# Optimization experiments

Measured on AMD Instinct MI355X. Metric: run time of the kernel, lower is better.

Reference implementation:

```python
import math
import jax, jax.numpy as jnp
import numpy as np

B, SX, SY, D, H = 2, 1024, 1024, 1024, 16
FULL = 1536   # padded (full_q == full_k) frame length for the two-source attention
N_CTX = 2048  # causal bias buffer size
HD = D // H
LENS_X = np.array([1024, 700])
LENS_Y = np.array([1024, 850])


def _heads(t):
    b, s, d = t.shape
    return t.reshape(b, s, H, HD).transpose(0, 2, 1, 3)  # [B,H,S,HD]


def _merge(t):
    b, h, s, hd = t.shape
    return t.transpose(0, 2, 1, 3).reshape(b, s, h * hd)


def setup_inputs() -> dict:
    key = jax.random.key(0)
    ks = jax.random.split(key, 8)
    s = 0.02
    # ragged pack/unpack index lists: take = positions in the FULL frame, fill = positions in the shrunk frame
    x_take_b = np.concatenate([np.full(l, b, np.int32) for b, l in enumerate(LENS_X)])
    x_take_p = np.concatenate([(FULL - l + np.arange(l)).astype(np.int32) for l in LENS_X])  # right-aligned
    x_fill_b = x_take_b.copy()
    x_fill_p = np.concatenate([np.arange(l, dtype=np.int32) for l in LENS_X])
    y_take_b = np.concatenate([np.full(l, b, np.int32) for b, l in enumerate(LENS_Y)])
    y_take_p = np.concatenate([np.arange(l, dtype=np.int32) for l in LENS_Y])  # left-aligned
    y_fill_b = y_take_b.copy()
    y_fill_p = y_take_p.copy()
    # additive padding mask for the self-attention over shrunk x
    mask = np.full((B, 1, 1, SX), -10000.0, np.float32)
    for b, l in enumerate(LENS_X):
        mask[b, :, :, :l] = 0.0
    return {
        "x": jax.random.normal(ks[0], (B, SX, D), jnp.float32),
        "y": jax.random.normal(ks[1], (B, SY, D), jnp.float32),
        "attention_mask_x": jnp.asarray(mask),
        "W_attn": jax.random.normal(ks[2], (D, 3 * D), jnp.float32) * s,
        "b_attn": jnp.zeros((3 * D,), jnp.float32),
        "W_2a": jax.random.normal(ks[3], (D, D), jnp.float32) * s,
        "b_2a": jnp.zeros((D,), jnp.float32),
        "W_2b": jax.random.normal(ks[4], (D, 2 * D), jnp.float32) * s,
        "b_2b": jnp.zeros((2 * D,), jnp.float32),
        "W_proj": jax.random.normal(ks[5], (2 * D, D), jnp.float32) * s,
        "b_proj": jnp.zeros((D,), jnp.float32),
        "x_take_b": jnp.asarray(x_take_b), "x_take_p": jnp.asarray(x_take_p),
        "x_fill_b": jnp.asarray(x_fill_b), "x_fill_p": jnp.asarray(x_fill_p),
        "y_take_b": jnp.asarray(y_take_b), "y_take_p": jnp.asarray(y_take_p),
        "y_fill_b": jnp.asarray(y_fill_b), "y_fill_p": jnp.asarray(y_fill_p),
    }


def reference(x, y, attention_mask_x, W_attn, b_attn, W_2a, b_2a, W_2b, b_2b,
              W_proj, b_proj, x_take_b, x_take_p, x_fill_b, x_fill_p,
              y_take_b, y_take_p, y_fill_b, y_fill_p):
    causal = jnp.tril(jnp.ones((N_CTX, N_CTX), jnp.float32))
    inv_sqrt = 1.0 / math.sqrt(HD)

    # --- branch 1: causal self-attention on shrunk x ---
    qkv = x @ W_attn + b_attn
    q, k, v = jnp.split(qkv, 3, axis=2)
    q, k, v = _heads(q), _heads(k), _heads(v)
    w = jnp.einsum('bhqd,bhkd->bhqk', q, k) * inv_sqrt  # [B,H,SX,SX]
    b1 = causal[:SX, :SX]
    w = w * b1 - 10000.0 * (1.0 - b1) + attention_mask_x
    a = jnp.einsum('bhqk,bhkd->bhqd', jax.nn.softmax(w, axis=-1), v)
    a = _merge(a)  # [B,SX,D]

    # --- branch 2: two-source attention with ragged expand/shrink ---
    q2 = _heads(x @ W_2a + b_2a)                      # [B,H,SX,HD]
    k2, v2 = jnp.split(y @ W_2b + b_2b, 2, axis=2)
    k2, v2 = _heads(k2), _heads(v2)                   # [B,H,SY,HD]
    w2 = jnp.einsum('bhqd,bhkd->bhqk', q2, k2)        # [B,H,SX,SY] (unscaled yet)
    # expand key dim: shrunk SY -> FULL
    temp = jnp.zeros((B, H, SX, FULL), w2.dtype)
    temp = temp.at[y_take_b, :, :, y_take_p].set(w2[y_fill_b, :, :, y_fill_p])
    # expand query dim: shrunk SX -> FULL
    new_w = jnp.zeros((B, H, FULL, FULL), w2.dtype)
    new_w = new_w.at[x_take_b, :, x_take_p, :].set(temp[x_fill_b, :, x_fill_p, :])
    new_v = jnp.zeros((B, H, FULL, HD), v2.dtype)
    new_v = new_v.at[y_take_b, :, y_take_p, :].set(v2[y_fill_b, :, y_fill_p, :])
    kmask = jnp.full((B, 1, 1, FULL), -10000.0, w2.dtype)
    kmask = kmask.at[y_take_b, :, :, y_take_p].set(0.0)
    new_w = new_w * inv_sqrt
    b2 = causal[:FULL, :FULL]  # ns-nd == 0 since full_q == full_k
    new_w = new_w * b2 - 10000.0 * (1.0 - b2) + kmask
    a2 = jnp.einsum('bhqk,bhkd->bhqd', jax.nn.softmax(new_w, axis=-1), new_v)  # [B,H,FULL,HD]
    # shrink query dim back: FULL -> SX
    a2s = jnp.zeros((B, H, SX, HD), a2.dtype)
    a2s = a2s.at[x_fill_b, :, x_fill_p, :].set(a2[x_take_b, :, x_take_p, :])
    a2m = _merge(a2s)  # [B,SX,D]

    out = jnp.concatenate([a, a2m], axis=2) @ W_proj + b_proj  # [B,SX,D]
    return out
```

## Files before the change

### kernel.cpp

```cpp
#include <hip/hip_runtime.h>
#include <hip/hip_bf16.h>

typedef __bf16 bf16;
typedef __attribute__((ext_vector_type(4))) __bf16 bf16x4;
typedef __attribute__((ext_vector_type(8))) __bf16 bf16x8;
typedef __attribute__((ext_vector_type(4))) float floatx4;

__device__ __forceinline__ void gl_lds16(const bf16* g, bf16* l) {
  __builtin_amdgcn_global_load_lds(
      (const __attribute__((address_space(1))) void*)g,
      (__attribute__((address_space(3))) void*)l, 16, 0, 0);
}

__global__ __launch_bounds__(256) void sentinel_kernel(float* out, int n, float code) {
  int i = blockIdx.x * 256 + threadIdx.x;
  if (i < n) out[i] = code;
}

struct TP { const float* W; bf16* WT; int K; int N; int bxn; int bid0; };

__global__ __launch_bounds__(256) void prep_kernel(TP t0, TP t1, TP t2, TP t3,
                                                   const float* __restrict__ x,
                                                   const float* __restrict__ y,
                                                   bf16* __restrict__ xb,
                                                   bf16* __restrict__ yb) {
  int bid = blockIdx.x;
  int tid = threadIdx.x;
  if (bid < 2048) {
    __shared__ float tile[64][65];
    TP t = t0;
    if (bid >= t3.bid0) t = t3;
    else if (bid >= t2.bid0) t = t2;
    else if (bid >= t1.bid0) t = t1;
    int rb = bid - t.bid0;
    int n0 = (rb % t.bxn) * 64, k0 = (rb / t.bxn) * 64;
    int tx = tid & 15, ty = tid >> 4;
#pragma unroll
    for (int i = 0; i < 4; ++i) {
      floatx4 v = *(const floatx4*)(t.W + (size_t)(k0 + ty + 16 * i) * t.N + n0 + tx * 4);
#pragma unroll
      for (int j = 0; j < 4; ++j) tile[ty + 16 * i][tx * 4 + j] = v[j];
    }
    __syncthreads();
#pragma unroll
    for (int i = 0; i < 4; ++i) {
      int nr = ty + 16 * i;
      bf16x4 o;
#pragma unroll
      for (int j = 0; j < 4; ++j) o[j] = (bf16)tile[tx * 4 + j][nr];
      *(bf16x4*)(t.WT + (size_t)(n0 + nr) * t.K + k0 + tx * 4) = o;
    }
  } else {
    long base = (long)(bid - 2048) * 4096 + (long)tid * 16;
    const float* src = x; bf16* dst = xb; long idx = base;
    if (base >= 2097152) { src = y; dst = yb; idx = base - 2097152; }
    floatx4 v0 = *(const floatx4*)(src + idx);
    floatx4 v1 = *(const floatx4*)(src + idx + 4);
    floatx4 v2 = *(const floatx4*)(src + idx + 8);
    floatx4 v3 = *(const floatx4*)(src + idx + 12);
    bf16x8 o0, o1;
#pragma unroll
    for (int i = 0; i < 4; ++i) {
      o0[i] = (bf16)v0[i]; o0[4 + i] = (bf16)v1[i];
      o1[i] = (bf16)v2[i]; o1[4 + i] = (bf16)v3[i];
    }
    *(bf16x8*)(dst + idx) = o0;
    *(bf16x8*)(dst + idx + 8) = o1;
  }
}

struct GP { const bf16* A; const bf16* WT; const float* bias; bf16* C; bf16* VT;
            int N; int ldc; int vcol0; int bxn; int bid0; };

__global__ __launch_bounds__(256, 3) void proj3_kernel(GP g0, GP g1, GP g2) {
  __shared__ __attribute__((aligned(16))) bf16 As[128 * 64];
  __shared__ __attribute__((aligned(16))) bf16 Bs[128 * 64];
  int rawb = blockIdx.x;
  int bid = (rawb & 7) * 96 + (rawb >> 3);
  GP g = g0;
  if (bid >= g2.bid0) g = g2;
  else if (bid >= g1.bid0) g = g1;
  int rb = bid - g.bid0;
  int row0 = (rb / g.bxn) * 128, col0 = (rb % g.bxn) * 128;
  int tid = threadIdx.x;
  int lane = tid & 63, wave = tid >> 6;
  int quad = lane >> 4, l16 = lane & 15;
  int wm = wave >> 1, wn = wave & 1;
  const bf16* Ag = g.A + (size_t)row0 * 1024;
  const bf16* Bg = g.WT + (size_t)col0 * 1024;

  floatx4 acc[4][4] = {};

  for (int k0 = 0; k0 < 1024; k0 += 64) {
#pragma unroll
    for (int s = 0; s < 4; ++s) {
      int sl = s * 256 + tid;
      int r = sl >> 3, o = sl & 7;
      int c = (o ^ (r & 7)) * 8;
      gl_lds16(Ag + (size_t)r * 1024 + k0 + c, As + (size_t)sl * 8);
      gl_lds16(Bg + (size_t)r * 1024 + k0 + c, Bs + (size_t)sl * 8);
    }
    __syncthreads();
#pragma unroll
    for (int kk = 0; kk < 2; ++kk) {
      int ko = kk * 4 + quad;
      bf16x8 afr[4], bfr[4];
#pragma unroll
      for (int r = 0; r < 4; ++r) {
        int m = wm * 64 + r * 16 + l16;
        afr[r] = *(const bf16x8*)(As + (size_t)(m * 8 + (ko ^ (m & 7))) * 8);
      }
#pragma unroll
      for (int c = 0; c < 4; ++c) {
        int n = wn * 64 + c * 16 + l16;
        bfr[c] = *(const bf16x8*)(Bs + (size_t)(n * 8 + (ko ^ (n & 7))) * 8);
      }
#pragma unroll
      for (int r = 0; r < 4; ++r)
#pragma unroll
        for (int c = 0; c < 4; ++c)
          acc[r][c] = __builtin_amdgcn_mfma_f32_16x16x32_bf16(afr[r], bfr[c], acc[r][c], 0, 0, 0);
    }
    __syncthreads();
  }

  int inV = (col0 >= g.vcol0);
  if (inV) {
#pragma unroll
    for (int c = 0; c < 4; ++c) {
      int gcol = col0 + wn * 64 + c * 16 + l16;
      float bv = g.bias[gcol];
      int vcol = gcol - g.vcol0;
      int hh = vcol >> 6, dd = vcol & 63;
#pragma unroll
      for (int r = 0; r < 4; ++r) {
        int row = row0 + wm * 64 + r * 16 + quad * 4;
        int bb = row >> 10, key = row & 1023;
        bf16x4 pk;
#pragma unroll
        for (int e = 0; e < 4; ++e) pk[e] = (bf16)(acc[r][c][e] + bv);
        *(bf16x4*)(g.VT + ((size_t)((bb << 4) + hh)) * 65536 + (size_t)dd * 1024 + key) = pk;
      }
    }
  } else {
    bf16* S = ((bf16*)As) + wave * 1152;
    float bvv[4];
#pragma unroll
    for (int c = 0; c < 4; ++c) bvv[c] = g.bias[col0 + wn * 64 + c * 16 + l16];
#pragma unroll
    for (int r = 0; r < 4; ++r) {
#pragma unroll
      for (int c = 0; c < 4; ++c)
#pragma unroll
        for (int e = 0; e < 4; ++e)
          S[(quad * 4 + e) * 72 + c * 16 + l16] = (bf16)(acc[r][c][e] + bvv[c]);
      asm volatile("s_waitcnt lgkmcnt(0)" ::: "memory");
      int R0 = row0 + wm * 64 + r * 16;
#pragma unroll
      for (int t = 0; t < 2; ++t) {
        int s = t * 64 + lane;
        int rr = s >> 3, q = s & 7;
        bf16x8 vv = *(const bf16x8*)(S + rr * 72 + q * 8);
        *(bf16x8*)(g.C + (size_t)(R0 + rr) * g.ldc + col0 + wn * 64 + q * 8) = vv;
      }
      asm volatile("s_waitcnt lgkmcnt(0)" ::: "memory");
    }
  }
}

__global__ __launch_bounds__(256) void gemm_out_kernel(const bf16* __restrict__ A,
                                                       const bf16* __restrict__ WT,
                                                       const float* __restrict__ bias,
                                                       float* __restrict__ C) {
  const int K = 2048;
  __shared__ __attribute__((aligned(16))) bf16 As[128 * 64];
  __shared__ __attribute__((aligned(16))) bf16 Bs[64 * 64];
  int raw = blockIdx.x;
  int bid = (raw & 7) * 32 + (raw >> 3);
  int row0 = (bid >> 4) * 128;
  int col0 = (bid & 15) * 64;
  int tid = threadIdx.x;
  int lane = tid & 63, wave = tid >> 6;
  int quad = lane >> 4, l16 = lane & 15;
  int wm = wave >> 1, wn = wave & 1;
  floatx4 acc[4][2] = {};
  for (int k0 = 0; k0 < K; k0 += 64) {
#pragma unroll
    for (int s = 0; s < 4; ++s) {
      int sl = s * 256 + tid;
      int r = sl >> 3, o = sl & 7;
      int c = (o ^ (r & 7)) * 8;
      gl_lds16(A + (size_t)(row0 + r) * K + k0 + c, As + (size_t)sl * 8);
      if (s < 2)
        gl_lds16(WT + (size_t)(col0 + r) * K + k0 + c, Bs + (size_t)sl * 8);
    }
    __syncthreads();
#pragma unroll
    for (int kk = 0; kk < 2; ++kk) {
      int ko = kk * 4 + quad;
      bf16x8 afr[4], bfr[2];
#pragma unroll
      for (int r = 0; r < 4; ++r) {
        int m = wm * 64 + r * 16 + l16;
        afr[r] = *(const bf16x8*)(As + (size_t)(m * 8 + (ko ^ (m & 7))) * 8);
      }
#pragma unroll
      for (int c = 0; c < 2; ++c) {
        int n = wn * 32 + c * 16 + l16;
        bfr[c] = *(const bf16x8*)(Bs + (size_t)(n * 8 + (ko ^ (n & 7))) * 8);
      }
#pragma unroll
      for (int r = 0; r < 4; ++r)
#pragma unroll
        for (int c = 0; c < 2; ++c)
          acc[r][c] = __builtin_amdgcn_mfma_f32_16x16x32_bf16(afr[r], bfr[c], acc[r][c], 0, 0, 0);
    }
    __syncthreads();
  }
#pragma unroll
  for (int c = 0; c < 2; ++c) {
    int gcol = col0 + wn * 32 + c * 16 + l16;
    float bv = bias[gcol];
#pragma unroll
    for (int r = 0; r < 4; ++r) {
      int grow = row0 + wm * 64 + r * 16 + quad * 4;
#pragma unroll
      for (int e = 0; e < 4; ++e)
        C[(size_t)(grow + e) * 1024 + gcol] = acc[r][c][e] + bv;
    }
  }
}

struct AP {
  const bf16* Q; const bf16* K; const bf16* VT; bf16* O;
  int qstride, kstride, ostride;
  long qbatch, kbatch, obatch;
  int coff0, coff1, klen0, klen1, qv0, qv1;
};

__global__ __launch_bounds__(512) void attn2x_kernel(AP a0, AP a1, float scale) {
  __shared__ __attribute__((aligned(16))) bf16 Ks[2][64 * 64];
  __shared__ __attribute__((aligned(16))) bf16 Vs[2][64 * 64];
  __shared__ __attribute__((aligned(16))) bf16 Ps[8][16 * 72];
  int grp = blockIdx.x >> 8;
  AP a = grp ? a1 : a0;
  int tid = threadIdx.x;
  int lane = tid & 63, w = tid >> 6;
  int quad = lane >> 4, l16 = lane & 15;
  int r = blockIdx.x & 255;
  int b = r >> 7, h = (r >> 3) & 15, qt = r & 7;
  if (grp) qt = 7 - qt;
  int coff = b ? a.coff1 : a.coff0;
  int klen = b ? a.klen1 : a.klen0;
  int qv = b ? a.qv1 : a.qv0;
  int qbase = qt * 128;
  int wq0 = qbase + w * 16;
  int qi = wq0 + l16;
  const bf16* Q   = a.Q + (size_t)b * a.qbatch + h * 64;
  const bf16* Kp  = a.K + (size_t)b * a.kbatch + h * 64;
  const bf16* VTp = a.VT + (size_t)(b * 16 + h) * 65536;
  bf16* O = a.O + (size_t)b * a.obatch + h * 64;

  bf16x8 aq0 = *(const bf16x8*)(Q + (size_t)qi * a.qstride + quad * 8);
  bf16x8 aq1 = *(const bf16x8*)(Q + (size_t)qi * a.qstride + 32 + quad * 8);

  floatx4 o[4] = {};
  float part = 0.f;

  int kend = klen < qbase + 128 + coff ? klen : qbase + 128 + coff;
  int nblk = (kend + 63) >> 6;
  int wkend0 = wq0 + 16 + coff;
  int wkend = klen < wkend0 ? klen : wkend0;

  const float KSC = scale * 1.44269504f;
  const float KOFF = -5.77078016f;

  auto stage = [&](int buf, int j0) {
    int row = tid >> 3, ch = tid & 7;
    gl_lds16(Kp + (size_t)(j0 + row) * a.kstride + ((ch ^ (row & 7)) * 8),
             Ks[buf] + (size_t)tid * 8);
    gl_lds16(VTp + (size_t)row * 1024 + j0 + ((ch ^ (row & 7)) * 8),
             Vs[buf] + (size_t)tid * 8);
  };

  stage(0, 0);
  for (int t = 0; t < nblk; ++t) {
    int j0 = t * 64;
    __syncthreads();
    if (t + 1 < nblk) stage((t + 1) & 1, j0 + 64);
    if (j0 >= wkend) continue;
    const bf16* Kt = Ks[t & 1];
    const bf16* Vt = Vs[t & 1];

    floatx4 sv[4];
    __builtin_amdgcn_s_setprio(1);
#pragma unroll
    for (int nt = 0; nt < 4; ++nt) {
      int key = nt * 16 + l16;
      int sl0 = key * 8 + (quad ^ (key & 7));
      int sl1 = key * 8 + ((quad + 4) ^ (key & 7));
      bf16x8 bk0 = *(const bf16x8*)(Kt + (size_t)sl0 * 8);
      bf16x8 bk1 = *(const bf16x8*)(Kt + (size_t)sl1 * 8);
      floatx4 z = {};
      z = __builtin_amdgcn_mfma_f32_16x16x32_bf16(bk0, aq0, z, 0, 0, 0);
      z = __builtin_amdgcn_mfma_f32_16x16x32_bf16(bk1, aq1, z, 0, 0, 0);
      sv[nt] = z;
    }
    __builtin_amdgcn_s_setprio(0);
    bool fullv = (j0 + 63 <= wq0 + coff) && (j0 + 63 < klen);
#pragma unroll
    for (int nt = 0; nt < 4; ++nt) {
      bf16x4 pk;
#pragma unroll
      for (int e = 0; e < 4; ++e) {
        float arg = fmaf(sv[nt][e], KSC, KOFF);
        if (!fullv) {
          int j = j0 + nt * 16 + quad * 4 + e;
          arg = (j <= qi + coff && j < klen) ? arg : -60.0f;
        }
        float p = exp2f(arg);
        part += p;
        pk[e] = (bf16)p;
      }
      *(bf16x4*)(Ps[w] + l16 * 72 + nt * 16 + quad * 4) = pk;
    }
    bf16x8 pb0 = *(const bf16x8*)(Ps[w] + l16 * 72 + quad * 8);
    bf16x8 pb1 = *(const bf16x8*)(Ps[w] + l16 * 72 + 32 + quad * 8);
    __builtin_amdgcn_s_setprio(1);
#pragma unroll
    for (int ct = 0; ct < 4; ++ct) {
      int dd = ct * 16 + l16;
      int sl0 = dd * 8 + (quad ^ (dd & 7));
      int sl1 = dd * 8 + ((quad + 4) ^ (dd & 7));
      bf16x8 va0 = *(const bf16x8*)(Vt + (size_t)sl0 * 8);
      bf16x8 va1 = *(const bf16x8*)(Vt + (size_t)sl1 * 8);
      o[ct] = __builtin_amdgcn_mfma_f32_16x16x32_bf16(va0, pb0, o[ct], 0, 0, 0);
      o[ct] = __builtin_amdgcn_mfma_f32_16x16x32_bf16(va1, pb1, o[ct], 0, 0, 0);
    }
    __builtin_amdgcn_s_setprio(0);
  }
  part += __shfl_xor(part, 16);
  part += __shfl_xor(part, 32);
  float rinv = 1.0f / part;
#pragma unroll
  for (int ct = 0; ct < 4; ++ct) {
    bf16x4 pk;
#pragma unroll
    for (int e = 0; e < 4; ++e) {
      float val = o[ct][e] * rinv;
      if (qi >= qv) val = 0.f;
      pk[e] = (bf16)val;
    }
    *(bf16x4*)(O + (size_t)qi * a.ostride + ct * 16 + quad * 4) = pk;
  }
}

extern "C" void kernel_launch(void* const* d_in, const int* in_sizes, int n_in,
                              void* d_out, int out_size, void* d_ws, size_t ws_size,
                              hipStream_t stream) {
  const float* x      = (const float*)d_in[0];
  const float* y      = (const float*)d_in[1];
  const float* W_attn = (const float*)d_in[3];
  const float* b_attn = (const float*)d_in[4];
  const float* W_2a   = (const float*)d_in[5];
  const float* b_2a   = (const float*)d_in[6];
  const float* W_2b   = (const float*)d_in[7];
  const float* b_2b   = (const float*)d_in[8];
  const float* W_proj = (const float*)d_in[9];
  const float* b_proj = (const float*)d_in[10];
  bf16* ws = (bf16*)d_ws;
  float* out = (float*)d_out;

  const int LX0 = 1024, LX1 = 700, LY0 = 1024, LY1 = 850;
  const float scale = 0.125f;
  const size_t WS_FAST = (size_t)25165824 * 2;

  if (ws_size < WS_FAST) {
    sentinel_kernel<<<(out_size + 255) / 256, 256, 0, stream>>>(
        out, out_size, (float)(ws_size >> 20) + 10.0f);
    return;
  }

  bf16* qk1  = ws;
  bf16* q2   = ws + (size_t) 4194304;
  bf16* k2   = ws + (size_t) 6291456;
  bf16* VT1  = ws + (size_t) 8388608;
  bf16* VT2  = ws + (size_t)10485760;
  bf16* xb   = ws + (size_t)12582912;
  bf16* yb   = ws + (size_t)14680064;
  bf16* cat  = ws + (size_t)12582912;
  bf16* WaT  = ws + (size_t)16777216;
  bf16* W2aT = ws + (size_t)19922944;
  bf16* W2bT = ws + (size_t)20971520;
  bf16* WpT  = ws + (size_t)23068672;

  TP t0 = {W_attn, WaT, 1024, 3072, 48, 0};
  TP t1 = {W_2a, W2aT, 1024, 1024, 16, 768};
  TP t2 = {W_2b, W2bT, 1024, 2048, 32, 1024};
  TP t3 = {W_proj, WpT, 2048, 1024, 16, 1536};
  prep_kernel<<<3072, 256, 0, stream>>>(t0, t1, t2, t3, x, y, xb, yb);

  GP g0 = {xb, WaT, b_attn, qk1, VT1, 3072, 2048, 2048, 24, 0};
  GP g1 = {xb, W2aT, b_2a, q2, nullptr, 1024, 1024, 1 << 30, 8, 384};
  GP g2 = {yb, W2bT, b_2b, k2, VT2, 2048, 1024, 1024, 16, 512};
  proj3_kernel<<<768, 256, 0, stream>>>(g0, g1, g2);

  AP a0 = {qk1, qk1 + 1024, VT1, cat, 2048, 2048, 2048,
           (long)1024 * 2048, (long)1024 * 2048, (long)1024 * 2048,
           0, 0, LX0, LX1, 1024, 1024};
  AP a1 = {q2, k2, VT2, cat + 1024, 1024, 1024, 2048,
           (long)1024 * 1024, (long)1024 * 1024, (long)1024 * 2048,
           1536 - LX0, 1536 - LX1, LY0, LY1, LX0, LX1};
  attn2x_kernel<<<512, 512, 0, stream>>>(a0, a1, scale);

  gemm_out_kernel<<<256, 256, 0, stream>>>(cat, WpT, b_proj, out);
}
```

Measured before the change: 216.7 us.

## Double-buffer output GEMM with smaller tiles and halve attention query tile

The output projection GEMM moves to 64x64 tiles with double-buffered LDS staging. The next K-slice is prefetched while MFMAs run, and the kernel launches 512 blocks instead of 256. The attention kernel now uses 64-query tiles with 256 threads and 1024 blocks, which gives finer causal load balance and more blocks across the CUs. The costs are more global reloads of K/V and weight tiles per output, and extra per-block overhead.

Measured after the change: 221.3 us. 2.1% more time.

```diff
diff --git a/kernel.cpp b/kernel.cpp
--- a/kernel.cpp
+++ b/kernel.cpp
@@ -173,60 +173,69 @@
                                                        const float* __restrict__ bias,
                                                        float* __restrict__ C) {
   const int K = 2048;
-  __shared__ __attribute__((aligned(16))) bf16 As[128 * 64];
-  __shared__ __attribute__((aligned(16))) bf16 Bs[64 * 64];
+  __shared__ __attribute__((aligned(16))) bf16 As[2][64 * 64];
+  __shared__ __attribute__((aligned(16))) bf16 Bs[2][64 * 64];
   int raw = blockIdx.x;
-  int bid = (raw & 7) * 32 + (raw >> 3);
-  int row0 = (bid >> 4) * 128;
+  int bid = (raw & 7) * 64 + (raw >> 3);
+  int row0 = (bid >> 4) * 64;
   int col0 = (bid & 15) * 64;
   int tid = threadIdx.x;
   int lane = tid & 63, wave = tid >> 6;
   int quad = lane >> 4, l16 = lane & 15;
-  int wm = wave >> 1, wn = wave & 1;
-  floatx4 acc[4][2] = {};
-  for (int k0 = 0; k0 < K; k0 += 64) {
-#pragma unroll
-    for (int s = 0; s < 4; ++s) {
-      int sl = s * 256 + tid;
-      int r = sl >> 3, o = sl & 7;
+
+  auto stage = [&](int buf, int k0) {
+#pragma unroll
+    for (int t = 0; t < 2; ++t) {
+      int i = t * 256 + tid;
+      int r = i >> 3, o = i & 7;
       int c = (o ^ (r & 7)) * 8;
-      gl_lds16(A + (size_t)(row0 + r) * K + k0 + c, As + (size_t)sl * 8);
-      if (s < 2)
-        gl_lds16(WT + (size_t)(col0 + r) * K + k0 + c, Bs + (size_t)sl * 8);
-    }
-    __syncthreads();
+      gl_lds16(A + (size_t)(row0 + r) * K + k0 + c, As[buf] + (size_t)i * 8);
+      gl_lds16(WT + (size_t)(col0 + r) * K + k0 + c, Bs[buf] + (size_t)i * 8);
+    }
+  };
+
+  floatx4 acc[4] = {};
+  stage(0, 0);
+  asm volatile("s_waitcnt vmcnt(0)" ::: "memory");
+  __builtin_amdgcn_s_barrier();
+
+  for (int T = 0; T < 32; ++T) {
+    int cb = T & 1, nb = cb ^ 1;
+    const bf16* Ac = As[cb];
+    const bf16* Bc = Bs[cb];
+    bf16x8 af[2], bf[2][4];
 #pragma unroll
     for (int kk = 0; kk < 2; ++kk) {
       int ko = kk * 4 + quad;
-      bf16x8 afr[4], bfr[2];
-#pragma unroll
-      for (int r = 0; r < 4; ++r) {
-        int m = wm * 64 + r * 16 + l16;
-        afr[r] = *(const bf16x8*)(As + (size_t)(m * 8 + (ko ^ (m & 7))) * 8);
-      }
-#pragma unroll
-      for (int c = 0; c < 2; ++c) {
-        int n = wn * 32 + c * 16 + l16;
-        bfr[c] = *(const bf16x8*)(Bs + (size_t)(n * 8 + (ko ^ (n & 7))) * 8);
-      }
-#pragma unroll
-      for (int r = 0; r < 4; ++r)
-#pragma unroll
-        for (int c = 0; c < 2; ++c)
-          acc[r][c] = __builtin_amdgcn_mfma_f32_16x16x32_bf16(afr[r], bfr[c], acc[r][c], 0, 0, 0);
-    }
-    __syncthreads();
-  }
-#pragma unroll
-  for (int c = 0; c < 2; ++c) {
-    int gcol = col0 + wn * 32 + c * 16 + l16;
+      int m = wave * 16 + l16;
+      af[kk] = *(const bf16x8*)(Ac + (size_t)(m * 8 + (ko ^ (m & 7))) * 8);
+#pragma unroll
+      for (int nt = 0; nt < 4; ++nt) {
+        int n = nt * 16 + l16;
+        bf[kk][nt] = *(const bf16x8*)(Bc + (size_t)(n * 8 + (ko ^ (n & 7))) * 8);
+      }
+    }
+    stage(nb, ((T + 1) & 31) * 64);
+    asm volatile("s_waitcnt lgkmcnt(0)" ::: "memory");
+    __builtin_amdgcn_sched_barrier(0);
+    __builtin_amdgcn_s_setprio(1);
+#pragma unroll
+    for (int kk = 0; kk < 2; ++kk)
+#pragma unroll
+      for (int nt = 0; nt < 4; ++nt)
+        acc[nt] = __builtin_amdgcn_mfma_f32_16x16x32_bf16(af[kk], bf[kk][nt], acc[nt], 0, 0, 0);
+    __builtin_amdgcn_s_setprio(0);
+    asm volatile("s_waitcnt vmcnt(0)" ::: "memory");
+    __builtin_amdgcn_s_barrier();
+  }
+#pragma unroll
+  for (int nt = 0; nt < 4; ++nt) {
+    int gcol = col0 + nt * 16 + l16;
     float bv = bias[gcol];
 #pragma unroll
-    for (int r = 0; r < 4; ++r) {
-      int grow = row0 + wm * 64 + r * 16 + quad * 4;
-#pragma unroll
-      for (int e = 0; e < 4; ++e)
-        C[(size_t)(grow + e) * 1024 + gcol] = acc[r][c][e] + bv;
+    for (int e = 0; e < 4; ++e) {
+      int grow = row0 + wave * 16 + quad * 4 + e;
+      C[(size_t)grow * 1024 + gcol] = acc[nt][e] + bv;
     }
   }
 }
@@ -238,22 +247,22 @@
   int coff0, coff1, klen0, klen1, qv0, qv1;
 };
 
-__global__ __launch_bounds__(512) void attn2x_kernel(AP a0, AP a1, float scale) {
+__global__ __launch_bounds__(256) void attn2x_kernel(AP a0, AP a1, float scale) {
   __shared__ __attribute__((aligned(16))) bf16 Ks[2][64 * 64];
   __shared__ __attribute__((aligned(16))) bf16 Vs[2][64 * 64];
-  __shared__ __attribute__((aligned(16))) bf16 Ps[8][16 * 72];
-  int grp = blockIdx.x >> 8;
+  __shared__ __attribute__((aligned(16))) bf16 Ps[4][16 * 72];
+  int grp = blockIdx.x >> 9;
   AP a = grp ? a1 : a0;
   int tid = threadIdx.x;
   int lane = tid & 63, w = tid >> 6;
   int quad = lane >> 4, l16 = lane & 15;
-  int r = blockIdx.x & 255;
-  int b = r >> 7, h = (r >> 3) & 15, qt = r & 7;
-  if (grp) qt = 7 - qt;
+  int r = blockIdx.x & 511;
+  int b = r >> 8, h = (r >> 4) & 15, qt = r & 15;
+  if (grp) qt = 15 - qt;
   int coff = b ? a.coff1 : a.coff0;
   int klen = b ? a.klen1 : a.klen0;
   int qv = b ? a.qv1 : a.qv0;
-  int qbase = qt * 128;
+  int qbase = qt * 64;
   int wq0 = qbase + w * 16;
   int qi = wq0 + l16;
   const bf16* Q   = a.Q + (size_t)b * a.qbatch + h * 64;
@@ -267,7 +276,7 @@
   floatx4 o[4] = {};
   float part = 0.f;
 
-  int kend = klen < qbase + 128 + coff ? klen : qbase + 128 + coff;
+  int kend = klen < qbase + 64 + coff ? klen : qbase + 64 + coff;
   int nblk = (kend + 63) >> 6;
   int wkend0 = wq0 + 16 + coff;
   int wkend = klen < wkend0 ? klen : wkend0;
@@ -276,11 +285,15 @@
   const float KOFF = -5.77078016f;
 
   auto stage = [&](int buf, int j0) {
-    int row = tid >> 3, ch = tid & 7;
-    gl_lds16(Kp + (size_t)(j0 + row) * a.kstride + ((ch ^ (row & 7)) * 8),
-             Ks[buf] + (size_t)tid * 8);
-    gl_lds16(VTp + (size_t)row * 1024 + j0 + ((ch ^ (row & 7)) * 8),
-             Vs[buf] + (size_t)tid * 8);
+#pragma unroll
+    for (int t = 0; t < 2; ++t) {
+      int i = t * 256 + tid;
+      int row = i >> 3, ch = i & 7;
+      gl_lds16(Kp + (size_t)(j0 + row) * a.kstride + ((ch ^ (row & 7)) * 8),
+               Ks[buf] + (size_t)i * 8);
+      gl_lds16(VTp + (size_t)row * 1024 + j0 + ((ch ^ (row & 7)) * 8),
+               Vs[buf] + (size_t)i * 8);
+    }
   };
 
   stage(0, 0);
@@ -411,7 +424,7 @@
   AP a1 = {q2, k2, VT2, cat + 1024, 1024, 1024, 2048,
            (long)1024 * 1024, (long)1024 * 1024, (long)1024 * 2048,
            1536 - LX0, 1536 - LX1, LY0, LY1, LX0, LX1};
-  attn2x_kernel<<<512, 512, 0, stream>>>(a0, a1, scale);
-
-  gemm_out_kernel<<<256, 256, 0, stream>>>(cat, WpT, b_proj, out);
-}
+  attn2x_kernel<<<1024, 256, 0, stream>>>(a0, a1, scale);
+
+  gemm_out_kernel<<<512, 256, 0, stream>>>(cat, WpT, b_proj, out);
+}
```
